# Optimization experiments

Hardware: AMD Instinct MI355X
Metric: run time of the kernel (lower is better)

## Reference

```python
import jax, jax.numpy as jnp
import numpy as np

DIM = 768
HEADS = 8
FRAMES = 9
B, T, N = 16, FRAMES, 1024
HEAD_DIM = DIM // HEADS
SCALE = HEAD_DIM ** -0.5


def setup_inputs() -> dict:
    key = jax.random.key(0)
    ks = jax.random.split(key, 6)
    s = lambda fan_in: 1.0 / np.sqrt(fan_in)
    return {
        "x": jax.random.normal(ks[0], (B, T, N, DIM), jnp.float32),
        "W_qkv": jax.random.normal(ks[1], (DIM, 3 * DIM), jnp.float32) * s(DIM),
        "W_temp": jax.random.normal(ks[2], (T, T), jnp.float32) * s(T),
        "b_temp": jax.random.normal(ks[3], (T,), jnp.float32) * s(T),
        "W_out": jax.random.normal(ks[4], (DIM, DIM), jnp.float32) * s(DIM),
        "b_out": jax.random.normal(ks[5], (DIM,), jnp.float32) * s(DIM),
    }


def reference(x, W_qkv, W_temp, b_temp, W_out, b_out):
    b, t, n, c = x.shape
    h, d = HEADS, HEAD_DIM
    qkv = x @ W_qkv  # (b,t,n,3c)
    q, k, v = jnp.split(qkv, 3, axis=-1)
    # 'b t n (h d) -> b h t n d'
    to_heads = lambda a: a.reshape(b, t, n, h, d).transpose(0, 3, 1, 2, 4)
    q, k, v = to_heads(q), to_heads(k), to_heads(v)
    # dots over d per spatial token, then mean over n: fuse mean into the contraction
    dots = jnp.einsum('bhtnd,bhsnd->bhts', q, k) * (SCALE / n)  # (b,h,t,s)
    attn = jax.nn.softmax(dots, axis=-1)
    # temporal_proj(attn.mean over heads): Linear on last dim s
    ta = attn.mean(axis=1) @ W_temp + b_temp  # (b,t,s)
    # broadcast over h,n,d: out[b,h,t,n,d] = sum_s ta[b,t,s] * v[b,h,s,n,d]
    out = jnp.einsum('bts,bhsnd->bhtnd', ta, v)
    out = out.transpose(0, 2, 3, 1, 4).reshape(b, t, n, c)  # 'b h t n d -> b t n (h d)'
    return out @ W_out + b_out
```

## Files before the change

kernel.cpp:

```cpp
#include <hip/hip_runtime.h>
#include <stdint.h>

typedef unsigned short u16;
typedef float f32x4 __attribute__((ext_vector_type(4)));
typedef short s16x8 __attribute__((ext_vector_type(8)));
typedef unsigned short u16x4 __attribute__((ext_vector_type(4)));

#define NB 16
#define NT 9
#define NN 1024
#define NDIM 768
#define NH 8
#define NHD 96
#define NM (NB*NT*NN)
#define NQK 1536
#define PLANE (NN*NDIM)
#define SCALE_F 0.10206207261596575f

typedef __attribute__((address_space(1))) const void gvoid_t;
typedef __attribute__((address_space(3))) void lvoid_t;
#define GLOAD_LDS16(gp, lp) __builtin_amdgcn_global_load_lds((gvoid_t*)(gp), (lvoid_t*)(lp), 16, 0, 0)

__device__ __forceinline__ unsigned f2bf_u(float x) {
    unsigned u = __builtin_bit_cast(unsigned, x);
    return (u + 0x7FFFu + ((u >> 16) & 1u)) >> 16;
}
__device__ __forceinline__ void cvt8(uint4 v, float* f) {
    f[0] = __builtin_bit_cast(float, v.x << 16);
    f[1] = __builtin_bit_cast(float, v.x & 0xFFFF0000u);
    f[2] = __builtin_bit_cast(float, v.y << 16);
    f[3] = __builtin_bit_cast(float, v.y & 0xFFFF0000u);
    f[4] = __builtin_bit_cast(float, v.z << 16);
    f[5] = __builtin_bit_cast(float, v.z & 0xFFFF0000u);
    f[6] = __builtin_bit_cast(float, v.w << 16);
    f[7] = __builtin_bit_cast(float, v.w & 0xFFFF0000u);
}
__device__ __forceinline__ uint4 pack8(const float* f) {
    uint4 o;
    o.x = f2bf_u(f[0]) | (f2bf_u(f[1]) << 16);
    o.y = f2bf_u(f[2]) | (f2bf_u(f[3]) << 16);
    o.z = f2bf_u(f[4]) | (f2bf_u(f[5]) << 16);
    o.w = f2bf_u(f[6]) | (f2bf_u(f[7]) << 16);
    return o;
}

__global__ void transpose_w(const float* __restrict__ Wqkv, u16* __restrict__ Wqkt) {
    __shared__ u16 t[32][33];
    int j0 = blockIdx.x * 32, c0 = blockIdx.y * 32;
    int tx = threadIdx.x, ty = threadIdx.y;
    t[ty][tx] = (u16)f2bf_u(Wqkv[(size_t)(c0 + ty) * 2304 + j0 + tx]);
    __syncthreads();
    Wqkt[(size_t)(j0 + ty) * 768 + c0 + tx] = t[tx][ty];
}

__global__ void wvo_gemm(const float* __restrict__ Wqkv, const float* __restrict__ Wout,
                         u16* __restrict__ Wvot) {
    __shared__ float la[32][33];
    __shared__ float lb[32][33];
    int c0 = blockIdx.x * 32, c20 = blockIdx.y * 32;
    int tx = threadIdx.x, ty = threadIdx.y;
    float acc = 0.f;
    for (int e0 = 0; e0 < 768; e0 += 32) {
        la[ty][tx] = Wout[(size_t)(e0 + ty) * 768 + c20 + tx];
        lb[ty][tx] = Wqkv[(size_t)(c0 + ty) * 2304 + 1536 + e0 + tx];
        __syncthreads();
        #pragma unroll
        for (int e = 0; e < 32; ++e)
            acc = fmaf(la[e][ty], lb[tx][e], acc);
        __syncthreads();
    }
    Wvot[(size_t)(c20 + ty) * 768 + c0 + tx] = (u16)f2bf_u(acc);
}

__global__ __launch_bounds__(256) void cvt_x(const float* __restrict__ x, u16* __restrict__ xb) {
    size_t i = (size_t)blockIdx.x * 256 + threadIdx.x;
    f32x4 v = ((const f32x4*)x)[i];
    u16x4 o;
    o.x = (u16)f2bf_u(v.x); o.y = (u16)f2bf_u(v.y);
    o.z = (u16)f2bf_u(v.z); o.w = (u16)f2bf_u(v.w);
    ((u16x4*)xb)[i] = o;
}

template<int WM>
__global__ __launch_bounds__(256, 2)
void gemm_bt(const u16* __restrict__ A, const u16* __restrict__ Bt,
             void* __restrict__ Cv, const float* __restrict__ bias,
             int M, int N, int K) {
    __shared__ __align__(16) u16 lA[128 * 64];
    __shared__ __align__(16) u16 lB[128 * 64];
    const int tid  = threadIdx.x;
    const int lane = tid & 63;
    const int nbx  = N >> 7;
    const int nb   = gridDim.x;
    const int cpx  = nb >> 3;
    const int bid  = blockIdx.x;
    const int swz  = (bid & 7) * cpx + (bid >> 3);
    const int bx   = swz % nbx, by = swz / nbx;
    const long m0  = (long)by << 7;
    const int n0   = bx << 7;
    const int wm   = ((tid >> 7) & 1) << 6;
    const int wn   = ((tid >> 6) & 1) << 6;

    f32x4 acc[4][4] = {};

    const int rA  = tid >> 3;
    const int seg = tid & 7;
    const u16* Ab = A + m0 * K + seg * 8;
    const u16* Bb = Bt + (long)n0 * K + seg * 8;
    u16* lAb = lA + (size_t)(tid & 192) * 8;
    u16* lBb = lB + (size_t)(tid & 192) * 8;

    const int ar = (wm + (lane & 15)) * 64 + (lane >> 4) * 8;
    const int br = (wn + (lane & 15)) * 64 + (lane >> 4) * 8;

    for (int k0 = 0; k0 < K; k0 += 64) {
        #pragma unroll
        for (int i = 0; i < 4; ++i) {
            GLOAD_LDS16(Ab + (size_t)(i * 32 + rA) * K + k0, lAb + i * 2048);
            GLOAD_LDS16(Bb + (size_t)(i * 32 + rA) * K + k0, lBb + i * 2048);
        }
        __syncthreads();
        #pragma unroll
        for (int kk = 0; kk < 64; kk += 32) {
            s16x8 af[4], bfr[4];
            #pragma unroll
            for (int mi = 0; mi < 4; ++mi)
                af[mi] = *(const s16x8*)&lA[ar + mi * 1024 + kk];
            #pragma unroll
            for (int ni = 0; ni < 4; ++ni)
                bfr[ni] = *(const s16x8*)&lB[br + ni * 1024 + kk];
            #pragma unroll
            for (int mi = 0; mi < 4; ++mi)
                #pragma unroll
                for (int ni = 0; ni < 4; ++ni)
                    acc[mi][ni] = __builtin_amdgcn_mfma_f32_16x16x32_bf16(
                        af[mi], bfr[ni], acc[mi][ni], 0, 0, 0);
        }
        __syncthreads();
    }

    const int crow = wm + ((lane >> 4) << 2);
    const int ccol = n0 + wn + (lane & 15);
    if constexpr (WM == 0) {
        u16* C = (u16*)Cv;
        #pragma unroll
        for (int mi = 0; mi < 4; ++mi)
            #pragma unroll
            for (int ni = 0; ni < 4; ++ni) {
                long r = m0 + crow + mi * 16;
                int  c = ccol + ni * 16;
                #pragma unroll
                for (int i = 0; i < 4; ++i)
                    C[(r + i) * (long)N + c] = (u16)f2bf_u(acc[mi][ni][i]);
            }
    } else {
        float* C = (float*)Cv;
        #pragma unroll
        for (int mi = 0; mi < 4; ++mi)
            #pragma unroll
            for (int ni = 0; ni < 4; ++ni) {
                long r = m0 + crow + mi * 16;
                int  c = ccol + ni * 16;
                float bv = bias[c];
                #pragma unroll
                for (int i = 0; i < 4; ++i)
                    C[(r + i) * (long)N + c] = acc[mi][ni][i] + bv;
            }
    }
}

__global__ __launch_bounds__(256)
void dots_partial(const u16* __restrict__ QK, float* __restrict__ part) {
    const int tid = threadIdx.x;
    const int ch  = blockIdx.x;
    const int h   = blockIdx.y;
    const int b   = blockIdx.z;
    const size_t tstride = (size_t)NN * NQK;
    const u16* base = QK + (size_t)b * 9 * tstride + h * NHD;

    float acc[9][9] = {};
    #pragma unroll 1
    for (int j = 0; j < 3; ++j) {
        int p  = ch * 768 + j * 256 + tid;
        int n  = p / 12, dc = p % 12;
        const u16* qp = base + (size_t)n * NQK + dc * 8;
        float qf[9][8];
        #pragma unroll
        for (int t = 0; t < 9; ++t) {
            uint4 qv = *(const uint4*)(qp + (size_t)t * tstride);
            cvt8(qv, qf[t]);
        }
        #pragma unroll
        for (int s = 0; s < 9; ++s) {
            uint4 kv = *(const uint4*)(qp + (size_t)s * tstride + 768);
            float kf[8]; cvt8(kv, kf);
            #pragma unroll
            for (int t = 0; t < 9; ++t)
                #pragma unroll
                for (int e = 0; e < 8; ++e)
                    acc[t][s] = fmaf(qf[t][e], kf[e], acc[t][s]);
        }
    }
    #pragma unroll
    for (int t = 0; t < 9; ++t)
        #pragma unroll
        for (int s = 0; s < 9; ++s) {
            float v = acc[t][s];
            #pragma unroll
            for (int m = 1; m < 64; m <<= 1) v += __shfl_xor(v, m, 64);
            acc[t][s] = v;
        }
    __shared__ float red[4][81];
    if ((tid & 63) == 0) {
        #pragma unroll
        for (int t = 0; t < 9; ++t)
            #pragma unroll
            for (int s = 0; s < 9; ++s) red[tid >> 6][t * 9 + s] = acc[t][s];
    }
    __syncthreads();
    if (tid < 81) {
        float v = red[0][tid] + red[1][tid] + red[2][tid] + red[3][tid];
        part[((size_t)ch * 128 + b * 8 + h) * 81 + tid] = v;
    }
}

__global__ void finalize_ta(const float* __restrict__ part, const float* __restrict__ Wtmp,
                            const float* __restrict__ btmp, float* __restrict__ ta) {
    const int b = blockIdx.x;
    const int tid = threadIdx.x;
    __shared__ float attn_l[8][9][9];
    if (tid < 72) {
        int h = tid / 9, t = tid % 9;
        float v[9];
        #pragma unroll
        for (int s = 0; s < 9; ++s) {
            float a = 0.f;
            for (int ch = 0; ch < 16; ++ch)
                a += part[((size_t)ch * 128 + b * 8 + h) * 81 + t * 9 + s];
            v[s] = a * (SCALE_F / 1024.0f);
        }
        float mx = v[0];
        #pragma unroll
        for (int s = 1; s < 9; ++s) mx = fmaxf(mx, v[s]);
        float den = 0.f;
        #pragma unroll
        for (int s = 0; s < 9; ++s) { v[s] = __expf(v[s] - mx); den += v[s]; }
        float inv = 1.0f / den;
        #pragma unroll
        for (int s = 0; s < 9; ++s) attn_l[h][t][s] = v[s] * inv;
    }
    __syncthreads();
    if (tid < 81) {
        int t = tid / 9, j = tid % 9;
        float o = btmp[j];
        #pragma unroll
        for (int s = 0; s < 9; ++s) {
            float am = 0.f;
            #pragma unroll
            for (int hh = 0; hh < 8; ++hh) am += attn_l[hh][t][s];
            o = fmaf(am * 0.125f, Wtmp[s * 9 + j], o);
        }
        ta[(size_t)b * 81 + t * 9 + j] = o;
    }
}

__global__ __launch_bounds__(256)
void tmix(u16* __restrict__ xb, const float* __restrict__ ta) {
    const int b = blockIdx.y;
    const int tid = threadIdx.x;
    __shared__ float tl[81];
    if (tid < 81) tl[tid] = ta[(size_t)b * 81 + tid];
    __syncthreads();
    size_t off = ((size_t)blockIdx.x * 256 + tid) * 8;
    u16* pb = xb + (size_t)b * 9 * PLANE + off;
    float acc[9][8] = {};
    #pragma unroll
    for (int s = 0; s < 9; ++s) {
        uint4 xv = *(const uint4*)(pb + (size_t)s * PLANE);
        float xf[8]; cvt8(xv, xf);
        #pragma unroll
        for (int t = 0; t < 9; ++t) {
            float w = tl[t * 9 + s];
            #pragma unroll
            for (int e = 0; e < 8; ++e) acc[t][e] = fmaf(w, xf[e], acc[t][e]);
        }
    }
    #pragma unroll
    for (int t = 0; t < 9; ++t)
        *(uint4*)(pb + (size_t)t * PLANE) = pack8(acc[t]);
}

extern "C" void kernel_launch(void* const* d_in, const int* in_sizes, int n_in,
                              void* d_out, int out_size, void* d_ws, size_t ws_size,
                              hipStream_t stream) {
    (void)in_sizes; (void)n_in; (void)out_size; (void)ws_size;
    const float* x    = (const float*)d_in[0];
    const float* Wqkv = (const float*)d_in[1];
    const float* Wtmp = (const float*)d_in[2];
    const float* btmp = (const float*)d_in[3];
    const float* Wout = (const float*)d_in[4];
    const float* bout = (const float*)d_in[5];

    char* ws = (char*)d_ws;
    u16*   xb   = (u16*)ws;
    u16*   Wqkt = (u16*)(ws + 226492416ull);
    u16*   Wvot = (u16*)(ws + 228851712ull);
    float* part = (float*)(ws + 230031360ull);
    float* ta   = (float*)(ws + 230694912ull);
    u16*   QK   = (u16*)d_out;

    transpose_w<<<dim3(48, 24), dim3(32, 32), 0, stream>>>(Wqkv, Wqkt);
    wvo_gemm<<<dim3(24, 24), dim3(32, 32), 0, stream>>>(Wqkv, Wout, Wvot);
    cvt_x<<<110592, 256, 0, stream>>>(x, xb);
    gemm_bt<0><<<13824, 256, 0, stream>>>(xb, Wqkt, (void*)QK, nullptr, NM, NQK, NDIM);
    dots_partial<<<dim3(16, 8, 16), 256, 0, stream>>>(QK, part);
    finalize_ta<<<16, 128, 0, stream>>>(part, Wtmp, btmp, ta);
    tmix<<<dim3(384, 16), 256, 0, stream>>>(xb, ta);
    gemm_bt<1><<<6912, 256, 0, stream>>>(xb, Wvot, d_out, bout, NM, NDIM, NDIM);
}
```

Measured before the change: 1.176 ms.

## Replace 128x128 GEMM with 256x256 tile, 4-stage LDS pipeline and swizzle

Both large GEMMs now use a 512-thread 256x256 tile kernel with a 4-deep ring of LDS buffers filled by direct global-to-LDS loads issued three k-steps ahead. Fine-grained vmcnt waits and barriers replace the per-iteration syncthreads, and an XOR swizzle is applied to LDS addresses to avoid bank conflicts. The goal is more reuse per loaded byte and overlap of memory traffic with MFMA work. In exchange it needs 128 KB of LDS and more accumulator registers, which may reduce occupancy, and the wait counts are hand-tuned with little margin for error.

```diff
diff --git a/kernel.cpp b/kernel.cpp
--- a/kernel.cpp
+++ b/kernel.cpp
@@ -81,74 +81,120 @@
     ((u16x4*)xb)[i] = o;
 }
 
+#define SWZ(a) ((a) ^ ((((a) >> 7) & 3) << 4))
 template<int WM>
-__global__ __launch_bounds__(256, 2)
-void gemm_bt(const u16* __restrict__ A, const u16* __restrict__ Bt,
-             void* __restrict__ Cv, const float* __restrict__ bias,
-             int M, int N, int K) {
-    __shared__ __align__(16) u16 lA[128 * 64];
-    __shared__ __align__(16) u16 lB[128 * 64];
+__global__ __launch_bounds__(512, 2)
+void gemm256(const u16* __restrict__ A, const u16* __restrict__ Bt,
+             void* __restrict__ Cv, const float* __restrict__ bias, int N) {
+    constexpr int K = 768;
+    constexpr int KT = 24;
+    __shared__ __align__(16) u16 lds[65536];
     const int tid  = threadIdx.x;
     const int lane = tid & 63;
-    const int nbx  = N >> 7;
-    const int nb   = gridDim.x;
-    const int cpx  = nb >> 3;
-    const int bid  = blockIdx.x;
-    const int swz  = (bid & 7) * cpx + (bid >> 3);
-    const int bx   = swz % nbx, by = swz / nbx;
-    const long m0  = (long)by << 7;
-    const int n0   = bx << 7;
-    const int wm   = ((tid >> 7) & 1) << 6;
-    const int wn   = ((tid >> 6) & 1) << 6;
-
-    f32x4 acc[4][4] = {};
-
-    const int rA  = tid >> 3;
-    const int seg = tid & 7;
-    const u16* Ab = A + m0 * K + seg * 8;
-    const u16* Bb = Bt + (long)n0 * K + seg * 8;
-    u16* lAb = lA + (size_t)(tid & 192) * 8;
-    u16* lBb = lB + (size_t)(tid & 192) * 8;
-
-    const int ar = (wm + (lane & 15)) * 64 + (lane >> 4) * 8;
-    const int br = (wn + (lane & 15)) * 64 + (lane >> 4) * 8;
-
-    for (int k0 = 0; k0 < K; k0 += 64) {
-        #pragma unroll
-        for (int i = 0; i < 4; ++i) {
-            GLOAD_LDS16(Ab + (size_t)(i * 32 + rA) * K + k0, lAb + i * 2048);
-            GLOAD_LDS16(Bb + (size_t)(i * 32 + rA) * K + k0, lBb + i * 2048);
-        }
-        __syncthreads();
-        #pragma unroll
-        for (int kk = 0; kk < 64; kk += 32) {
-            s16x8 af[4], bfr[4];
-            #pragma unroll
-            for (int mi = 0; mi < 4; ++mi)
-                af[mi] = *(const s16x8*)&lA[ar + mi * 1024 + kk];
-            #pragma unroll
-            for (int ni = 0; ni < 4; ++ni)
-                bfr[ni] = *(const s16x8*)&lB[br + ni * 1024 + kk];
+    const int wid  = tid >> 6;
+    const int wr   = wid >> 2;
+    const int wc   = wid & 3;
+    const int nbx  = N >> 8;
+    const int cpx  = (int)gridDim.x >> 3;
+    const int bid  = (int)blockIdx.x;
+    const int swzb = (bid & 7) * cpx + (bid >> 3);
+    const int bx   = swzb % nbx, by = swzb / nbx;
+    const long m0  = (long)by << 8;
+    const long n0  = (long)bx << 8;
+
+    const u16 *ag0, *ag1, *bg0, *bg1;
+    u16 *ad0, *ad1, *bd0, *bd1;
+    {
+        int a0 = tid * 16, a1 = 8192 + tid * 16;
+        int p0 = SWZ(a0), p1 = SWZ(a1);
+        ag0 = A  + (m0 + (p0 >> 6)) * K + ((p0 & 63) >> 1);
+        ag1 = A  + (m0 + (p1 >> 6)) * K + ((p1 & 63) >> 1);
+        bg0 = Bt + (n0 + (p0 >> 6)) * K + ((p0 & 63) >> 1);
+        bg1 = Bt + (n0 + (p1 >> 6)) * K + ((p1 & 63) >> 1);
+        u16* wbase = (u16*)lds + (size_t)(tid & ~63) * 8;
+        ad0 = wbase;          ad1 = wbase + 4096;
+        bd0 = wbase + 8192;   bd1 = wbase + 12288;
+    }
+
+    int aoff[8], boff[4];
+    #pragma unroll
+    for (int mi = 0; mi < 8; ++mi) {
+        int row = wr * 128 + mi * 16 + (lane & 15);
+        int byt = row * 64 + ((lane >> 4) << 4);
+        aoff[mi] = SWZ(byt);
+    }
+    #pragma unroll
+    for (int ni = 0; ni < 4; ++ni) {
+        int row = wc * 64 + ni * 16 + (lane & 15);
+        int byt = row * 64 + ((lane >> 4) << 4);
+        boff[ni] = 16384 + SWZ(byt);
+    }
+
+    f32x4 acc[8][4] = {};
+
+    #define STAGE_A(tt) { const int b_ = ((tt) & 3) * 16384; const int k_ = (tt) * 32; \
+        GLOAD_LDS16(ag0 + k_, ad0 + b_); GLOAD_LDS16(ag1 + k_, ad1 + b_); }
+    #define STAGE_B(tt) { const int b_ = ((tt) & 3) * 16384; const int k_ = (tt) * 32; \
+        GLOAD_LDS16(bg0 + k_, bd0 + b_); GLOAD_LDS16(bg1 + k_, bd1 + b_); }
+
+    STAGE_A(0); STAGE_B(0);
+    STAGE_A(1); STAGE_B(1);
+    STAGE_A(2); STAGE_B(2);
+    asm volatile("s_waitcnt vmcnt(8)" ::: "memory");
+    __builtin_amdgcn_s_barrier();
+
+    for (int t = 0; t < KT; ++t) {
+        const char* lp = (const char*)lds + ((t & 3) << 15);
+        s16x8 bf[4];
+        {
+            s16x8 af[4];
+            #pragma unroll
+            for (int mi = 0; mi < 4; ++mi) af[mi] = *(const s16x8*)(lp + aoff[mi]);
+            #pragma unroll
+            for (int ni = 0; ni < 4; ++ni) bf[ni] = *(const s16x8*)(lp + boff[ni]);
+            if (t + 3 < KT) STAGE_A(t + 3);
+            __builtin_amdgcn_s_setprio(1);
             #pragma unroll
             for (int mi = 0; mi < 4; ++mi)
                 #pragma unroll
                 for (int ni = 0; ni < 4; ++ni)
                     acc[mi][ni] = __builtin_amdgcn_mfma_f32_16x16x32_bf16(
-                        af[mi], bfr[ni], acc[mi][ni], 0, 0, 0);
-        }
-        __syncthreads();
-    }
-
-    const int crow = wm + ((lane >> 4) << 2);
-    const int ccol = n0 + wn + (lane & 15);
+                        af[mi], bf[ni], acc[mi][ni], 0, 0, 0);
+            __builtin_amdgcn_s_setprio(0);
+        }
+        __builtin_amdgcn_s_barrier();
+        {
+            s16x8 af[4];
+            #pragma unroll
+            for (int mi = 0; mi < 4; ++mi) af[mi] = *(const s16x8*)(lp + aoff[4 + mi]);
+            if (t + 3 < KT) STAGE_B(t + 3);
+            __builtin_amdgcn_s_setprio(1);
+            #pragma unroll
+            for (int mi = 0; mi < 4; ++mi)
+                #pragma unroll
+                for (int ni = 0; ni < 4; ++ni)
+                    acc[4 + mi][ni] = __builtin_amdgcn_mfma_f32_16x16x32_bf16(
+                        af[mi], bf[ni], acc[4 + mi][ni], 0, 0, 0);
+            __builtin_amdgcn_s_setprio(0);
+        }
+        if (t < KT - 3)       { asm volatile("s_waitcnt vmcnt(8)" ::: "memory"); }
+        else if (t == KT - 3) { asm volatile("s_waitcnt vmcnt(4)" ::: "memory"); }
+        else if (t == KT - 2) { asm volatile("s_waitcnt vmcnt(0)" ::: "memory"); }
+        __builtin_amdgcn_s_barrier();
+    }
+    #undef STAGE_A
+    #undef STAGE_B
+
+    const int crow = (lane >> 4) << 2;
+    const int ccol = lane & 15;
     if constexpr (WM == 0) {
         u16* C = (u16*)Cv;
         #pragma unroll
-        for (int mi = 0; mi < 4; ++mi)
+        for (int mi = 0; mi < 8; ++mi)
             #pragma unroll
             for (int ni = 0; ni < 4; ++ni) {
-                long r = m0 + crow + mi * 16;
-                int  c = ccol + ni * 16;
+                long r = m0 + wr * 128 + mi * 16 + crow;
+                long c = n0 + wc * 64 + ni * 16 + ccol;
                 #pragma unroll
                 for (int i = 0; i < 4; ++i)
                     C[(r + i) * (long)N + c] = (u16)f2bf_u(acc[mi][ni][i]);
@@ -156,11 +202,11 @@
     } else {
         float* C = (float*)Cv;
         #pragma unroll
-        for (int mi = 0; mi < 4; ++mi)
+        for (int mi = 0; mi < 8; ++mi)
             #pragma unroll
             for (int ni = 0; ni < 4; ++ni) {
-                long r = m0 + crow + mi * 16;
-                int  c = ccol + ni * 16;
+                long r = m0 + wr * 128 + mi * 16 + crow;
+                long c = n0 + wc * 64 + ni * 16 + ccol;
                 float bv = bias[c];
                 #pragma unroll
                 for (int i = 0; i < 4; ++i)
@@ -312,9 +358,9 @@
     transpose_w<<<dim3(48, 24), dim3(32, 32), 0, stream>>>(Wqkv, Wqkt);
     wvo_gemm<<<dim3(24, 24), dim3(32, 32), 0, stream>>>(Wqkv, Wout, Wvot);
     cvt_x<<<110592, 256, 0, stream>>>(x, xb);
-    gemm_bt<0><<<13824, 256, 0, stream>>>(xb, Wqkt, (void*)QK, nullptr, NM, NQK, NDIM);
+    gemm256<0><<<3456, 512, 0, stream>>>(xb, Wqkt, (void*)QK, nullptr, NQK);
     dots_partial<<<dim3(16, 8, 16), 256, 0, stream>>>(QK, part);
     finalize_ta<<<16, 128, 0, stream>>>(part, Wtmp, btmp, ta);
     tmix<<<dim3(384, 16), 256, 0, stream>>>(xb, ta);
-    gemm_bt<1><<<6912, 256, 0, stream>>>(xb, Wvot, d_out, bout, NM, NDIM, NDIM);
-}
+    gemm256<1><<<1728, 512, 0, stream>>>(xb, Wvot, d_out, bout, NDIM);
+}
```

New measurement: 1.023 ms. 13.0% less time.
